# Kernel tuning notes

Hardware: AMD Instinct MI355X
Metric: run time of the kernel (lower is better)

Reference implementation:

```python
import jax, jax.numpy as jnp
import numpy as np
from jax import lax

IN_CH, OUT_CH, K = 64, 64, 3
FAN_IN = 8           # LogicNets-style fan-in per output channel (over C_in*K taps)
IN_SCALE, IN_BITS = 0.0625, 8
OUT_SCALE, OUT_BITS = 0.125, 8


def make_mask(seed=7):
    # Binary mask [OUT_CH, IN_CH, K] with exactly FAN_IN ones per output channel
    rng = np.random.RandomState(seed)
    m = np.zeros((OUT_CH, IN_CH * K), dtype=np.float32)
    for o in range(OUT_CH):
        idx = rng.choice(IN_CH * K, size=FAN_IN, replace=False)
        m[o, idx] = 1.0
    return jnp.asarray(m.reshape(OUT_CH, IN_CH, K))


def fake_quant(v, scale, bits):
    # symmetric fake quantization with straight-through estimator
    qmin = -(2 ** (bits - 1))
    qmax = 2 ** (bits - 1) - 1
    q = jnp.clip(jnp.round(v / scale), qmin, qmax) * scale
    return v + lax.stop_gradient(q - v)


def setup_inputs() -> dict:
    key = jax.random.key(0)
    k1, k2 = jax.random.split(key)
    x = jax.random.normal(k1, (512, IN_CH, 1024), dtype=jnp.float32)
    weight = jax.random.normal(k2, (OUT_CH, IN_CH, K), dtype=jnp.float32) * 0.1
    mask = make_mask()
    return {"x": x, "weight": weight, "mask": mask}


def reference(x, weight, mask):
    # input quant
    xq = fake_quant(x, IN_SCALE, IN_BITS)
    # masked (sparse) conv1d, padding=1 (same length)
    w = weight * mask
    out = lax.conv_general_dilated(
        xq, w,
        window_strides=(1,),
        padding=[(1, 1)],
        dimension_numbers=("NCH", "OIH", "NCH"),
    )
    # output quant
    return fake_quant(out, OUT_SCALE, OUT_BITS)
```

## Files before the change

### kernel.cpp

```cpp
#include <hip/hip_runtime.h>

namespace {
constexpr int kInCh  = 64;
constexpr int kOutCh = 64;
constexpr int kK     = 3;
constexpr int kFanIn = 8;
constexpr int kH     = 1024;
constexpr int kTile  = 64;
constexpr int kRow   = kTile + 8;
constexpr int kBlk   = 256;
constexpr int kHB    = kH / kTile;
}

struct Tap { int off; float w; };

__device__ __forceinline__ float quant_in_i(float v) {
    float q = rintf(v * 16.0f);
    q = fmaxf(q, -128.0f);
    return fminf(q, 127.0f);
}

__device__ __forceinline__ float quant_out(float v) {
    float q = rintf(v * 8.0f);
    q = fmaxf(q, -128.0f);
    q = fminf(q, 127.0f);
    return q * 0.125f;
}

__global__ void prep_taps(const float* __restrict__ weight,
                          const float* __restrict__ mask,
                          Tap* __restrict__ taps) {
    __shared__ unsigned long long bal[3];
    const int o    = blockIdx.x;
    const int j    = threadIdx.x;
    const int k    = j >> 6;
    const int ci   = j & 63;
    const int idx  = (o * kInCh + ci) * kK + k;

    const float m = mask[idx];
    const unsigned long long b = __ballot(m != 0.0f);
    if (ci == 0) bal[k] = b;
    __syncthreads();

    const unsigned long long lower = b & ((1ull << ci) - 1ull);
    int rank = __popcll(lower);
    #pragma unroll
    for (int w = 0; w < kK; ++w) if (w < k) rank += __popcll(bal[w]);

    if (m != 0.0f && rank < kFanIn) {
        taps[o * kFanIn + rank].off = ci * kRow + k + 3;
        taps[o * kFanIn + rank].w   = weight[idx] * m * 0.0625f;
    }
    int total = __popcll(bal[0]) + __popcll(bal[1]) + __popcll(bal[2]);
    if (j >= total && j < kFanIn) {
        taps[o * kFanIn + j].off = 3;
        taps[o * kFanIn + j].w   = 0.0f;
    }
}

__global__ __launch_bounds__(kBlk, 8) void sparse_conv(
        const float* __restrict__ x,
        const Tap*   __restrict__ taps,
        float*       __restrict__ out) {
    __shared__ float sm[kInCh * kRow];

    const int t    = threadIdx.x;
    const int lane = t & 63;
    const int g    = __builtin_amdgcn_readfirstlane(t >> 6);
    const int h0   = blockIdx.x * kTile;
    const int n    = blockIdx.y;
    const float* __restrict__ xn = x + (size_t)n * kInCh * kH + h0;

    float4 r[4];
    #pragma unroll
    for (int it = 0; it < 4; ++it) {
        const int f  = it * kBlk + t;
        const int ci = f >> 4;
        const int c4 = f & 15;
        r[it] = reinterpret_cast<const float4*>(xn + ci * kH)[c4];
    }
    float hv = 0.f;
    if (t < 64) {
        if (h0 > 0) hv = xn[t * kH - 1];
    } else if (t < 128) {
        if (h0 + kTile < kH) hv = xn[(t - 64) * kH + kTile];
    }

    #pragma unroll
    for (int it = 0; it < 4; ++it) {
        const int f  = it * kBlk + t;
        const int ci = f >> 4;
        const int c4 = f & 15;
        float4 q;
        q.x = quant_in_i(r[it].x); q.y = quant_in_i(r[it].y);
        q.z = quant_in_i(r[it].z); q.w = quant_in_i(r[it].w);
        reinterpret_cast<float4*>(&sm[ci * kRow + 4])[c4] = q;
    }
    if (t < 64) {
        sm[t * kRow + 3] = quant_in_i(hv);
    } else if (t < 128) {
        sm[(t - 64) * kRow + 4 + kTile] = quant_in_i(hv);
    }
    __syncthreads();

    float* __restrict__ outn = out + (size_t)n * kOutCh * kH + h0;

    #pragma unroll 4
    for (int oo = 0; oo < 16; ++oo) {
        const int o = g * 16 + oo;
        const Tap* __restrict__ tp = taps + o * kFanIn;
        float acc = 0.f;
        #pragma unroll
        for (int j = 0; j < kFanIn; ++j) {
            acc = fmaf(tp[j].w, sm[tp[j].off + lane], acc);
        }
        outn[o * kH + lane] = quant_out(acc);
    }
}

extern "C" void kernel_launch(void* const* d_in, const int* in_sizes, int n_in,
                              void* d_out, int out_size, void* d_ws, size_t ws_size,
                              hipStream_t stream) {
    const float* x      = (const float*)d_in[0];
    const float* weight = (const float*)d_in[1];
    const float* mask   = (const float*)d_in[2];
    float* out = (float*)d_out;
    Tap* taps = (Tap*)d_ws;

    const int nBatch = in_sizes[0] / (kInCh * kH);

    prep_taps<<<kOutCh, kInCh * kK, 0, stream>>>(weight, mask, taps);
    dim3 grid(kHB, nBatch);
    sparse_conv<<<grid, kBlk, 0, stream>>>(x, taps, out);
}
```

Baseline: 238.1 us.

## Make conv kernel persistent with per-wave tiles and register-prefetched next tile

Replaces the one-block-per-tile grid with a persistent grid of 512 blocks. Each wave independently owns a whole 64x64 input tile in its own shared-memory slice and computes all 64 output channels for it. While computing the current tile, each wave prefetches the next tile into 16 float4 registers, which removes block-wide barriers and overlaps global loads with compute. The cost is much higher register pressure (64 floats of prefetch per lane), four times the LDS per block, and lower occupancy, with launch bounds dropped to 2.

```diff
diff --git a/kernel.cpp b/kernel.cpp
--- a/kernel.cpp
+++ b/kernel.cpp
@@ -7,9 +7,11 @@
 constexpr int kFanIn = 8;
 constexpr int kH     = 1024;
 constexpr int kTile  = 64;
-constexpr int kRow   = kTile + 8;
-constexpr int kBlk   = 256;
+constexpr int kRow   = 72;
+constexpr int kWaves = 4;
+constexpr int kBlk   = 64 * kWaves;
 constexpr int kHB    = kH / kTile;
+constexpr int kGridB = 512;
 }
 
 struct Tap { int off; float w; };
@@ -58,63 +60,72 @@
     }
 }
 
-__global__ __launch_bounds__(kBlk, 8) void sparse_conv(
+__device__ __forceinline__ void issue_loads(const float* __restrict__ x, int tau,
+                                            int lane, float4* __restrict__ r,
+                                            float& hl, float& hr) {
+    const int n  = tau >> 4;
+    const int h0 = (tau & (kHB - 1)) * kTile;
+    const float* __restrict__ p = x + ((size_t)n * kInCh) * kH + h0;
+    #pragma unroll
+    for (int i = 0; i < 16; ++i) {
+        const int f = i * 64 + lane;
+        r[i] = reinterpret_cast<const float4*>(p + (f >> 4) * kH)[f & 15];
+    }
+    hl = 0.f; hr = 0.f;
+    if (h0 > 0)          hl = p[lane * kH - 1];
+    if (h0 + kTile < kH) hr = p[lane * kH + kTile];
+}
+
+__device__ __forceinline__ void stage(float (* __restrict__ my)[kRow], int lane,
+                                      const float4* __restrict__ r, float hl, float hr) {
+    #pragma unroll
+    for (int i = 0; i < 16; ++i) {
+        const int f = i * 64 + lane;
+        float4 q;
+        q.x = quant_in_i(r[i].x); q.y = quant_in_i(r[i].y);
+        q.z = quant_in_i(r[i].z); q.w = quant_in_i(r[i].w);
+        *reinterpret_cast<float4*>(&my[f >> 4][4 + (f & 15) * 4]) = q;
+    }
+    my[lane][3]         = quant_in_i(hl);
+    my[lane][4 + kTile] = quant_in_i(hr);
+}
+
+__global__ __launch_bounds__(kBlk, 2) void sparse_conv(
         const float* __restrict__ x,
         const Tap*   __restrict__ taps,
-        float*       __restrict__ out) {
-    __shared__ float sm[kInCh * kRow];
+        float*       __restrict__ out,
+        int nTiles, int strideW) {
+    __shared__ float sm[kWaves][kInCh][kRow];
 
     const int t    = threadIdx.x;
     const int lane = t & 63;
     const int g    = __builtin_amdgcn_readfirstlane(t >> 6);
-    const int h0   = blockIdx.x * kTile;
-    const int n    = blockIdx.y;
-    const float* __restrict__ xn = x + (size_t)n * kInCh * kH + h0;
+    float (* __restrict__ my)[kRow] = sm[g];
+    const float* __restrict__ smf = &my[0][0];
 
-    float4 r[4];
-    #pragma unroll
-    for (int it = 0; it < 4; ++it) {
-        const int f  = it * kBlk + t;
-        const int ci = f >> 4;
-        const int c4 = f & 15;
-        r[it] = reinterpret_cast<const float4*>(xn + ci * kH)[c4];
-    }
-    float hv = 0.f;
-    if (t < 64) {
-        if (h0 > 0) hv = xn[t * kH - 1];
-    } else if (t < 128) {
-        if (h0 + kTile < kH) hv = xn[(t - 64) * kH + kTile];
-    }
+    int tau = blockIdx.x * kWaves + g;
+    float4 r[16]; float hl, hr;
+    if (tau < nTiles) issue_loads(x, tau, lane, r, hl, hr);
 
-    #pragma unroll
-    for (int it = 0; it < 4; ++it) {
-        const int f  = it * kBlk + t;
-        const int ci = f >> 4;
-        const int c4 = f & 15;
-        float4 q;
-        q.x = quant_in_i(r[it].x); q.y = quant_in_i(r[it].y);
-        q.z = quant_in_i(r[it].z); q.w = quant_in_i(r[it].w);
-        reinterpret_cast<float4*>(&sm[ci * kRow + 4])[c4] = q;
-    }
-    if (t < 64) {
-        sm[t * kRow + 3] = quant_in_i(hv);
-    } else if (t < 128) {
-        sm[(t - 64) * kRow + 4 + kTile] = quant_in_i(hv);
-    }
-    __syncthreads();
+    while (tau < nTiles) {
+        stage(my, lane, r, hl, hr);
+        const int cur = tau;
+        tau += strideW;
+        if (tau < nTiles) issue_loads(x, tau, lane, r, hl, hr);
 
-    float* __restrict__ outn = out + (size_t)n * kOutCh * kH + h0;
+        const int n  = cur >> 4;
+        const int h0 = (cur & (kHB - 1)) * kTile;
+        float* __restrict__ outn = out + ((size_t)n * kOutCh) * kH + h0;
 
-    #pragma unroll 4
-    for (int oo = 0; oo < 16; ++oo) {
-        const int o = g * 16 + oo;
-        const Tap* __restrict__ tp = taps + o * kFanIn;
-        float acc = 0.f;
-        #pragma unroll
-        for (int j = 0; j < kFanIn; ++j) {
-            acc = fmaf(tp[j].w, sm[tp[j].off + lane], acc);
+        #pragma unroll 8
+        for (int o = 0; o < kOutCh; ++o) {
+            const Tap* __restrict__ tp = taps + o * kFanIn;
+            float acc = 0.f;
+            #pragma unroll
+            for (int j = 0; j < kFanIn; ++j)
+                acc = fmaf(tp[j].w, smf[tp[j].off + lane], acc);
+            outn[(size_t)o * kH + lane] = quant_out(acc);
         }
-        outn[o * kH + lane] = quant_out(acc);
     }
 }
 
@@ -128,8 +139,9 @@
     Tap* taps = (Tap*)d_ws;
 
     const int nBatch = in_sizes[0] / (kInCh * kH);
+    const int nTiles = nBatch * kHB;
+    const int strideW = kGridB * kWaves;
 
     prep_taps<<<kOutCh, kInCh * kK, 0, stream>>>(weight, mask, taps);
-    dim3 grid(kHB, nBatch);
-    sparse_conv<<<grid, kBlk, 0, stream>>>(x, taps, out);
+    sparse_conv<<<kGridB, kBlk, 0, stream>>>(x, taps, out, nTiles, strideW);
 }
```

Result: slower. 255.6 us (+7.4%).

## Drop LDS staging; gather sparse taps directly from global with vector loads

Applied to the files above, without the earlier changes.

Replaces the shared-memory tile of quantized inputs with direct unaligned 4-wide global loads per tap, so each thread computes four output positions across a 256-wide tile. Per-channel tap shifts are packed into a bitmask so that only the edge tiles need special boundary handling, done through templated variants. This removes the LDS fill, the block barrier and the full-tile quantization of all 64 input channels. In exchange, inputs are re-read and re-quantized from global/L2 once per tap use, with misaligned vector accesses.

```diff
diff --git a/kernel.cpp b/kernel.cpp
--- a/kernel.cpp
+++ b/kernel.cpp
@@ -6,13 +6,14 @@
 constexpr int kK     = 3;
 constexpr int kFanIn = 8;
 constexpr int kH     = 1024;
-constexpr int kTile  = 64;
-constexpr int kRow   = kTile + 8;
-constexpr int kBlk   = 256;
-constexpr int kHB    = kH / kTile;
+constexpr int kTileH = 256;
+constexpr int kBlk   = 512;
+constexpr int kHB    = kH / kTileH;
 }
 
-struct Tap { int off; float w; };
+struct Tap { int rel; float w; };
+
+typedef float f4u __attribute__((ext_vector_type(4), aligned(4)));
 
 __device__ __forceinline__ float quant_in_i(float v) {
     float q = rintf(v * 16.0f);
@@ -29,14 +30,17 @@
 
 __global__ void prep_taps(const float* __restrict__ weight,
                           const float* __restrict__ mask,
-                          Tap* __restrict__ taps) {
+                          Tap* __restrict__ taps,
+                          unsigned* __restrict__ dks) {
     __shared__ unsigned long long bal[3];
+    __shared__ unsigned sdk;
     const int o    = blockIdx.x;
     const int j    = threadIdx.x;
     const int k    = j >> 6;
     const int ci   = j & 63;
     const int idx  = (o * kInCh + ci) * kK + k;
 
+    if (j == 0) sdk = 0u;
     const float m = mask[idx];
     const unsigned long long b = __ballot(m != 0.0f);
     if (ci == 0) bal[k] = b;
@@ -48,74 +52,84 @@
     for (int w = 0; w < kK; ++w) if (w < k) rank += __popcll(bal[w]);
 
     if (m != 0.0f && rank < kFanIn) {
-        taps[o * kFanIn + rank].off = ci * kRow + k + 3;
+        taps[o * kFanIn + rank].rel = ci * kH + (k - 1);
         taps[o * kFanIn + rank].w   = weight[idx] * m * 0.0625f;
+        atomicOr(&sdk, (unsigned)k << (2 * rank));
     }
     int total = __popcll(bal[0]) + __popcll(bal[1]) + __popcll(bal[2]);
     if (j >= total && j < kFanIn) {
-        taps[o * kFanIn + j].off = 3;
+        taps[o * kFanIn + j].rel = 0;
         taps[o * kFanIn + j].w   = 0.0f;
+        atomicOr(&sdk, 1u << (2 * j));
+    }
+    __syncthreads();
+    if (j == 0) dks[o] = sdk;
+}
+
+template <int EDGE>
+__device__ __forceinline__ void conv_body(const float* __restrict__ xn,
+                                          const Tap* __restrict__ taps,
+                                          const unsigned* __restrict__ dks,
+                                          float* __restrict__ outn,
+                                          int h0, int g, int lane) {
+    const int hb = lane << 2;
+    const float* __restrict__ xr = xn + h0;
+
+    #pragma unroll 1
+    for (int oo = 0; oo < 8; ++oo) {
+        const int o = g * 8 + oo;
+        const Tap* __restrict__ tp = taps + o * kFanIn;
+        const unsigned dk8 = dks[o];
+        float a0 = 0.f, a1 = 0.f, a2 = 0.f, a3 = 0.f;
+
+        #pragma unroll
+        for (int j = 0; j < kFanIn; ++j) {
+            const int   rel = tp[j].rel;
+            const float w   = tp[j].w;
+            f4u v;
+            if (EDGE == 0) {
+                v = *reinterpret_cast<const f4u*>(xr + rel + hb);
+            } else {
+                const int dk = (int)((dk8 >> (2 * j)) & 3u) - 1;
+                if (EDGE < 0 && dk == -1) {
+                    const bool bad = (hb == 0);
+                    v = *reinterpret_cast<const f4u*>(xr + rel + hb + (bad ? 1 : 0));
+                    if (bad) { v.w = v.z; v.z = v.y; v.y = v.x; v.x = 0.f; }
+                } else if (EDGE > 0 && dk == 1) {
+                    const bool bad = (hb == kTileH - 4);
+                    v = *reinterpret_cast<const f4u*>(xr + rel + hb - (bad ? 1 : 0));
+                    if (bad) { v.x = v.y; v.y = v.z; v.z = v.w; v.w = 0.f; }
+                } else {
+                    v = *reinterpret_cast<const f4u*>(xr + rel + hb);
+                }
+            }
+            a0 = fmaf(w, quant_in_i(v.x), a0);
+            a1 = fmaf(w, quant_in_i(v.y), a1);
+            a2 = fmaf(w, quant_in_i(v.z), a2);
+            a3 = fmaf(w, quant_in_i(v.w), a3);
+        }
+        float4 q = make_float4(quant_out(a0), quant_out(a1), quant_out(a2), quant_out(a3));
+        *reinterpret_cast<float4*>(outn + (size_t)o * kH + h0 + hb) = q;
     }
 }
 
 __global__ __launch_bounds__(kBlk, 8) void sparse_conv(
         const float* __restrict__ x,
         const Tap*   __restrict__ taps,
+        const unsigned* __restrict__ dks,
         float*       __restrict__ out) {
-    __shared__ float sm[kInCh * kRow];
-
     const int t    = threadIdx.x;
     const int lane = t & 63;
     const int g    = __builtin_amdgcn_readfirstlane(t >> 6);
-    const int h0   = blockIdx.x * kTile;
+    const int hb   = blockIdx.x;
     const int n    = blockIdx.y;
-    const float* __restrict__ xn = x + (size_t)n * kInCh * kH + h0;
+    const int h0   = hb * kTileH;
+    const float* __restrict__ xn   = x   + (size_t)n * kInCh  * kH;
+    float*       __restrict__ outn = out + (size_t)n * kOutCh * kH;
 
-    float4 r[4];
-    #pragma unroll
-    for (int it = 0; it < 4; ++it) {
-        const int f  = it * kBlk + t;
-        const int ci = f >> 4;
-        const int c4 = f & 15;
-        r[it] = reinterpret_cast<const float4*>(xn + ci * kH)[c4];
-    }
-    float hv = 0.f;
-    if (t < 64) {
-        if (h0 > 0) hv = xn[t * kH - 1];
-    } else if (t < 128) {
-        if (h0 + kTile < kH) hv = xn[(t - 64) * kH + kTile];
-    }
-
-    #pragma unroll
-    for (int it = 0; it < 4; ++it) {
-        const int f  = it * kBlk + t;
-        const int ci = f >> 4;
-        const int c4 = f & 15;
-        float4 q;
-        q.x = quant_in_i(r[it].x); q.y = quant_in_i(r[it].y);
-        q.z = quant_in_i(r[it].z); q.w = quant_in_i(r[it].w);
-        reinterpret_cast<float4*>(&sm[ci * kRow + 4])[c4] = q;
-    }
-    if (t < 64) {
-        sm[t * kRow + 3] = quant_in_i(hv);
-    } else if (t < 128) {
-        sm[(t - 64) * kRow + 4 + kTile] = quant_in_i(hv);
-    }
-    __syncthreads();
-
-    float* __restrict__ outn = out + (size_t)n * kOutCh * kH + h0;
-
-    #pragma unroll 4
-    for (int oo = 0; oo < 16; ++oo) {
-        const int o = g * 16 + oo;
-        const Tap* __restrict__ tp = taps + o * kFanIn;
-        float acc = 0.f;
-        #pragma unroll
-        for (int j = 0; j < kFanIn; ++j) {
-            acc = fmaf(tp[j].w, sm[tp[j].off + lane], acc);
-        }
-        outn[o * kH + lane] = quant_out(acc);
-    }
+    if (hb == 0)              conv_body<-1>(xn, taps, dks, outn, h0, g, lane);
+    else if (hb == kHB - 1)   conv_body< 1>(xn, taps, dks, outn, h0, g, lane);
+    else                      conv_body< 0>(xn, taps, dks, outn, h0, g, lane);
 }
 
 extern "C" void kernel_launch(void* const* d_in, const int* in_sizes, int n_in,
@@ -125,11 +139,12 @@
     const float* weight = (const float*)d_in[1];
     const float* mask   = (const float*)d_in[2];
     float* out = (float*)d_out;
-    Tap* taps = (Tap*)d_ws;
+    Tap*      taps = (Tap*)d_ws;
+    unsigned* dks  = (unsigned*)(taps + kOutCh * kFanIn);
 
     const int nBatch = in_sizes[0] / (kInCh * kH);
 
-    prep_taps<<<kOutCh, kInCh * kK, 0, stream>>>(weight, mask, taps);
+    prep_taps<<<kOutCh, kInCh * kK, 0, stream>>>(weight, mask, taps, dks);
     dim3 grid(kHB, nBatch);
-    sparse_conv<<<grid, kBlk, 0, stream>>>(x, taps, out);
+    sparse_conv<<<grid, kBlk, 0, stream>>>(x, taps, dks, out);
 }
```

Measured after the change: 310.3 us. 30.3% more time.
